# Kernel tuning notes

Hardware: AMD Instinct MI355X
Metric: run time of the kernel (lower is better)

Reference implementation:

```python
import jax, jax.numpy as jnp
import numpy as np

HASH_BINS = 100000
EMB = 64
B = 262144


def _glorot(key, shape):
    fan_in, fan_out = shape[0], shape[-1]
    std = np.sqrt(2.0 / (fan_in + fan_out)).astype(np.float32)
    return jax.random.normal(key, shape, dtype=jnp.float32) * std


def setup_inputs() -> dict:
    key = jax.random.key(0)
    ks = jax.random.split(key, 16)
    return {
        "user_idx": jax.random.randint(ks[0], (B,), 0, HASH_BINS, dtype=jnp.int32),
        "item_idx": jax.random.randint(ks[1], (B,), 0, HASH_BINS, dtype=jnp.int32),
        "user_emb": jax.random.normal(ks[2], (HASH_BINS, EMB), dtype=jnp.float32) * 0.05,
        "item_emb": jax.random.normal(ks[3], (HASH_BINS, EMB), dtype=jnp.float32) * 0.05,
        "lin_w": jax.random.normal(ks[4], (2 * HASH_BINS,), dtype=jnp.float32) * 0.01,
        "lin_b": jnp.zeros((1,), jnp.float32),
        "cross_k": _glorot(ks[5], (2 * EMB, 2 * EMB)),
        "W1": _glorot(ks[6], (2 * EMB, 200)), "b1": jnp.zeros((200,), jnp.float32),
        "W2": _glorot(ks[7], (200, 256)),     "b2": jnp.zeros((256,), jnp.float32),
        "W3": _glorot(ks[8], (256, 200)),     "b3": jnp.zeros((200,), jnp.float32),
        "W4": _glorot(ks[9], (200, 128)),     "b4": jnp.zeros((128,), jnp.float32),
        "W5": _glorot(ks[10], (128, 1)),      "b5": jnp.zeros((1,), jnp.float32),
    }


def reference(user_idx, item_idx, user_emb, item_emb, lin_w, lin_b, cross_k,
              W1, b1, W2, b2, W3, b3, W4, b4, W5, b5):
    # Embedding lookups (flattened + concatenated): [B, 2*EMB]
    emb = jnp.concatenate([user_emb[user_idx], item_emb[item_idx]], axis=1)

    # FM linear term. CategoryEncoding(multi-hot over 2*HASH_BINS) -> Dense(1)
    # is exactly a gather-sum of the dense kernel rows (one user + one item token).
    linear = (lin_w[user_idx] + lin_w[HASH_BINS + item_idx] + lin_b)[:, None]  # [B,1]

    # FM cross term: 0.5 * mean((xK)^2 - x^2 K^2, axis=1)
    xk = emb @ cross_k                      # [B, 128]
    x2k2 = (emb * emb) @ (cross_k * cross_k)
    cross = 0.5 * jnp.mean(xk * xk - x2k2, axis=1, keepdims=True)  # [B,1]

    # Deep MLP (inference: no dropout)
    h = jax.nn.relu(emb @ W1 + b1)
    h = jax.nn.relu(h @ W2 + b2)
    h = jax.nn.relu(h @ W3 + b3)
    h = jax.nn.relu(h @ W4 + b4)
    dnn = h @ W5 + b5                       # [B,1]

    return jax.nn.sigmoid(linear + cross + dnn)
```

## Files before the change

kernel.cpp:

```cpp
#include <hip/hip_runtime.h>

#define HASH_BINS 100000
#define EMBD 64
#define BATCH 262144
#define BM 64
#define SA 264
#define SB 232

typedef __attribute__((ext_vector_type(8))) short short8;
typedef __attribute__((ext_vector_type(4))) float floatx4;
typedef __attribute__((ext_vector_type(4))) unsigned short ushortx4;

static __device__ __forceinline__ unsigned short f2bf(float f) {
  unsigned u = __builtin_bit_cast(unsigned, f);
  u += 0x7fff + ((u >> 16) & 1);
  return (unsigned short)(u >> 16);
}
static __device__ __forceinline__ float bf2f(unsigned short b) {
  return __builtin_bit_cast(float, ((unsigned)b) << 16);
}

__global__ void dfm_prep(const float* __restrict__ K, const float* __restrict__ W1,
                         const float* __restrict__ W2, const float* __restrict__ W3,
                         const float* __restrict__ W4,
                         float* __restrict__ S, unsigned short* __restrict__ Kt,
                         unsigned short* __restrict__ W1t, unsigned short* __restrict__ W2t,
                         unsigned short* __restrict__ W3t, unsigned short* __restrict__ W4t)
{
  int i = blockIdx.x * 256 + threadIdx.x;
  if (i < 4096) {
    int n = i >> 5, k4 = (i & 31) * 4;
    ushortx4 h = { f2bf(K[(k4 + 0) * 128 + n]), f2bf(K[(k4 + 1) * 128 + n]),
                   f2bf(K[(k4 + 2) * 128 + n]), f2bf(K[(k4 + 3) * 128 + n]) };
    *(ushortx4*)&Kt[n * 128 + k4] = h;
  } else if ((i -= 4096) < 7168) {
    int n = i >> 5, k4 = (i & 31) * 4;
    ushortx4 h;
#pragma unroll
    for (int j = 0; j < 4; j++) h[j] = (n < 200) ? f2bf(W1[(k4 + j) * 200 + n]) : 0;
    *(ushortx4*)&W1t[n * 128 + k4] = h;
  } else if ((i -= 7168) < 14336) {
    int n = i / 56, k4 = (i - n * 56) * 4;
    ushortx4 h;
#pragma unroll
    for (int j = 0; j < 4; j++) h[j] = (k4 + j < 200) ? f2bf(W2[(k4 + j) * 256 + n]) : 0;
    *(ushortx4*)&W2t[n * 224 + k4] = h;
  } else if ((i -= 14336) < 14336) {
    int n = i >> 6, k4 = (i & 63) * 4;
    ushortx4 h;
#pragma unroll
    for (int j = 0; j < 4; j++) h[j] = (n < 200) ? f2bf(W3[(k4 + j) * 200 + n]) : 0;
    *(ushortx4*)&W3t[n * 256 + k4] = h;
  } else if ((i -= 14336) < 7168) {
    int n = i / 56, k4 = (i - n * 56) * 4;
    ushortx4 h;
#pragma unroll
    for (int j = 0; j < 4; j++) h[j] = (k4 + j < 200) ? f2bf(W4[(k4 + j) * 128 + n]) : 0;
    *(ushortx4*)&W4t[n * 224 + k4] = h;
  } else if ((i -= 7168) < 128) {
    float s = 0.f;
    for (int j = 0; j < 128; j++) { float v = K[i * 128 + j]; s += v * v; }
    S[i] = s;
  }
}

template <int KP, int CH>
static __device__ __forceinline__ void wpref(const unsigned short* __restrict__ wt,
                                             int tileRow0, int m, int qd, short8* wpre)
{
#pragma unroll
  for (int n = 0; n < CH; n++)
    wpre[n] = *(const short8*)&wt[(tileRow0 + n * 16 + m) * KP + qd * 8];
}

template <int KP, int CH>
static __device__ __forceinline__ void mfma_pass_pre(const unsigned short* __restrict__ wt,
                                                     int tileRow0, const unsigned short* actIn,
                                                     int sin, int m, int qd, floatx4* acc,
                                                     const short8* wpre)
{
#pragma unroll
  for (int i = 0; i < CH * 4; i++) acc[i] = {0.f, 0.f, 0.f, 0.f};
  short8 a[4];
#pragma unroll
  for (int rt = 0; rt < 4; rt++)
    a[rt] = *(const short8*)&actIn[(rt * 16 + m) * sin + qd * 8];
#pragma unroll
  for (int n = 0; n < CH; n++)
#pragma unroll
    for (int rt = 0; rt < 4; rt++)
      acc[n * 4 + rt] = __builtin_amdgcn_mfma_f32_16x16x32_bf16(wpre[n], a[rt], acc[n * 4 + rt], 0, 0, 0);
#pragma unroll
  for (int ks = 1; ks < KP / 32; ks++) {
#pragma unroll
    for (int rt = 0; rt < 4; rt++)
      a[rt] = *(const short8*)&actIn[(rt * 16 + m) * sin + ks * 32 + qd * 8];
#pragma unroll
    for (int n = 0; n < CH; n++) {
      short8 w = *(const short8*)&wt[(tileRow0 + n * 16 + m) * KP + ks * 32 + qd * 8];
#pragma unroll
      for (int rt = 0; rt < 4; rt++)
        acc[n * 4 + rt] = __builtin_amdgcn_mfma_f32_16x16x32_bf16(w, a[rt], acc[n * 4 + rt], 0, 0, 0);
    }
  }
}

template <int KP, int CH>
static __device__ __forceinline__ void mfma_pass(const unsigned short* __restrict__ wt,
                                                 int tileRow0, const unsigned short* actIn,
                                                 int sin, int m, int qd, floatx4* acc)
{
#pragma unroll
  for (int i = 0; i < CH * 4; i++) acc[i] = {0.f, 0.f, 0.f, 0.f};
#pragma unroll
  for (int ks = 0; ks < KP / 32; ks++) {
    short8 a[4];
#pragma unroll
    for (int rt = 0; rt < 4; rt++)
      a[rt] = *(const short8*)&actIn[(rt * 16 + m) * sin + ks * 32 + qd * 8];
#pragma unroll
    for (int n = 0; n < CH; n++) {
      short8 w = *(const short8*)&wt[(tileRow0 + n * 16 + m) * KP + ks * 32 + qd * 8];
#pragma unroll
      for (int rt = 0; rt < 4; rt++)
        acc[n * 4 + rt] = __builtin_amdgcn_mfma_f32_16x16x32_bf16(w, a[rt], acc[n * 4 + rt], 0, 0, 0);
    }
  }
}

template <int CH>
static __device__ __forceinline__ void epilogue_relu(const float* __restrict__ bias,
                                                     int colBase, int nreal,
                                                     unsigned short* actOut, int sout,
                                                     int m, int qd, const floatx4* acc)
{
#pragma unroll
  for (int n = 0; n < CH; n++) {
    int col = colBase + n * 16 + qd * 4;
    float b0 = 0.f, b1 = 0.f, b2 = 0.f, b3 = 0.f;
    if (col < nreal) {
      float4 q = *(const float4*)(bias + col);
      b0 = q.x; b1 = q.y; b2 = q.z; b3 = q.w;
    }
#pragma unroll
    for (int rt = 0; rt < 4; rt++) {
      ushortx4 h = { f2bf(fmaxf(acc[n * 4 + rt][0] + b0, 0.f)),
                     f2bf(fmaxf(acc[n * 4 + rt][1] + b1, 0.f)),
                     f2bf(fmaxf(acc[n * 4 + rt][2] + b2, 0.f)),
                     f2bf(fmaxf(acc[n * 4 + rt][3] + b3, 0.f)) };
      *(ushortx4*)&actOut[(rt * 16 + m) * sout + col] = h;
    }
  }
}

__global__ __launch_bounds__(512)
void dfm_main(const int* __restrict__ uidx, const int* __restrict__ iidx,
              const float* __restrict__ uemb, const float* __restrict__ iemb,
              const float* __restrict__ linw, const float* __restrict__ linb,
              const float* __restrict__ b1, const float* __restrict__ b2,
              const float* __restrict__ b3, const float* __restrict__ b4,
              const float* __restrict__ W5, const float* __restrict__ b5,
              const float* __restrict__ S, const unsigned short* __restrict__ Wc,
              const unsigned short* __restrict__ W2t, const unsigned short* __restrict__ W3t,
              const unsigned short* __restrict__ W4t,
              float* __restrict__ out)
{
  __shared__ unsigned short actA[BM * SA];
  __shared__ unsigned short actB[BM * SB];
  __shared__ float crosspart[4][BM];
  __shared__ float part[BM][8];
  __shared__ float qpart[BM][8];
  __shared__ float linrow[BM];

  const int t = threadIdx.x;
  const int lane = t & 63, wave = t >> 6;
  const int m = lane & 15, qd = lane >> 4;
  const int r = t >> 3, c = t & 7;

  {
    int g = blockIdx.x * BM + r;
    int u = uidx[g], it = iidx[g];
    const float* up = uemb + (long)u * EMBD + c * 8;
    const float* ip = iemb + (long)it * EMBD + c * 8;
    float qp = 0.f;
#pragma unroll
    for (int j = 0; j < 8; j += 4) {
      float4 f = *(const float4*)(up + j);
      int col = c * 8 + j;
      float4 sv = *(const float4*)(S + col);
      ushortx4 h = {f2bf(f.x), f2bf(f.y), f2bf(f.z), f2bf(f.w)};
      *(ushortx4*)&actA[r * SA + col] = h;
      qp += f.x * f.x * sv.x + f.y * f.y * sv.y + f.z * f.z * sv.z + f.w * f.w * sv.w;
    }
#pragma unroll
    for (int j = 0; j < 8; j += 4) {
      float4 f = *(const float4*)(ip + j);
      int col = 64 + c * 8 + j;
      float4 sv = *(const float4*)(S + col);
      ushortx4 h = {f2bf(f.x), f2bf(f.y), f2bf(f.z), f2bf(f.w)};
      *(ushortx4*)&actA[r * SA + col] = h;
      qp += f.x * f.x * sv.x + f.y * f.y * sv.y + f.z * f.z * sv.z + f.w * f.w * sv.w;
    }
    qpart[r][c] = qp;
    if (c == 0) linrow[r] = linw[u] + linw[HASH_BINS + it] + linb[0];
  }

  short8 wpre[3];
  if (wave < 4)      wpref<128, 2>(Wc, 2 * wave * 16, m, qd, wpre);
  else if (wave < 6) wpref<128, 3>(Wc, 128 + (4 + (wave - 4) * 3) * 16, m, qd, wpre);
  else               wpref<128, 2>(Wc, 128 + (10 + (wave - 6) * 2) * 16, m, qd, wpre);
  __syncthreads();

  if (wave < 4) {
    floatx4 acc[8];
    mfma_pass_pre<128, 2>(Wc, 2 * wave * 16, actA, SA, m, qd, acc, wpre);
    float s[4];
#pragma unroll
    for (int rt = 0; rt < 4; rt++) {
      s[rt] = 0.f;
#pragma unroll
      for (int n = 0; n < 2; n++)
#pragma unroll
        for (int i = 0; i < 4; i++)
          s[rt] += acc[n * 4 + rt][i] * acc[n * 4 + rt][i];
      s[rt] += __shfl_xor(s[rt], 16, 64);
      s[rt] += __shfl_xor(s[rt], 32, 64);
    }
    if (qd == 0)
#pragma unroll
      for (int rt = 0; rt < 4; rt++)
        crosspart[wave][rt * 16 + m] = s[rt];
    floatx4 acc2[4];
    mfma_pass<128, 1>(Wc, 128 + wave * 16, actA, SA, m, qd, acc2);
    epilogue_relu<1>(b1, wave * 16, 200, actB, SB, m, qd, acc2);
  } else if (wave < 6) {
    int s0 = 4 + (wave - 4) * 3;
    floatx4 acc[12];
    mfma_pass_pre<128, 3>(Wc, 128 + s0 * 16, actA, SA, m, qd, acc, wpre);
    epilogue_relu<3>(b1, s0 * 16, 200, actB, SB, m, qd, acc);
  } else {
    int s0 = 10 + (wave - 6) * 2;
    floatx4 acc[8];
    mfma_pass_pre<128, 2>(Wc, 128 + s0 * 16, actA, SA, m, qd, acc, wpre);
    epilogue_relu<2>(b1, s0 * 16, 200, actB, SB, m, qd, acc);
  }
  wpref<224, 2>(W2t, wave * 32, m, qd, wpre);
  __syncthreads();

  {
    floatx4 acc[8];
    mfma_pass_pre<224, 2>(W2t, wave * 32, actB, SB, m, qd, acc, wpre);
    epilogue_relu<2>(b2, wave * 32, 256, actA, SA, m, qd, acc);
  }
  if (wave < 6) wpref<256, 2>(W3t, wave * 32, m, qd, wpre);
  else          wpref<256, 1>(W3t, (12 + (wave - 6)) * 16, m, qd, wpre);
  __syncthreads();

  if (wave < 6) {
    floatx4 acc[8];
    mfma_pass_pre<256, 2>(W3t, wave * 32, actA, SA, m, qd, acc, wpre);
    epilogue_relu<2>(b3, wave * 32, 200, actB, SB, m, qd, acc);
  } else {
    int s0 = (12 + (wave - 6)) * 16;
    floatx4 acc[4];
    mfma_pass_pre<256, 1>(W3t, s0, actA, SA, m, qd, acc, wpre);
    epilogue_relu<1>(b3, s0, 200, actB, SB, m, qd, acc);
  }
  wpref<224, 1>(W4t, wave * 16, m, qd, wpre);
  __syncthreads();

  {
    floatx4 acc[4];
    mfma_pass_pre<224, 1>(W4t, wave * 16, actB, SB, m, qd, acc, wpre);
    int nb = wave * 16 + qd * 4;
    float4 w5q = *(const float4*)(W5 + nb);
    float4 b4q = *(const float4*)(b4 + nb);
#pragma unroll
    for (int rt = 0; rt < 4; rt++) {
      float s = fmaxf(acc[rt][0] + b4q.x, 0.f) * w5q.x +
                fmaxf(acc[rt][1] + b4q.y, 0.f) * w5q.y +
                fmaxf(acc[rt][2] + b4q.z, 0.f) * w5q.z +
                fmaxf(acc[rt][3] + b4q.w, 0.f) * w5q.w;
      s += __shfl_xor(s, 16, 64);
      s += __shfl_xor(s, 32, 64);
      if (qd == 0) part[rt * 16 + m][wave] = s;
    }
  }
  __syncthreads();

  if (t < BM) {
    int rr = t;
    float xk2 = crosspart[0][rr] + crosspart[1][rr] + crosspart[2][rr] + crosspart[3][rr];
    float qs = qpart[rr][0] + qpart[rr][1] + qpart[rr][2] + qpart[rr][3] +
               qpart[rr][4] + qpart[rr][5] + qpart[rr][6] + qpart[rr][7];
    float dnn = part[rr][0] + part[rr][1] + part[rr][2] + part[rr][3] +
                part[rr][4] + part[rr][5] + part[rr][6] + part[rr][7];
    const float inv = 0.5f / 128.f;
    float logit = linrow[rr] + inv * (xk2 - qs) + dnn + b5[0];
    out[blockIdx.x * BM + rr] = 1.f / (1.f + expf(-logit));
  }
}

extern "C" void kernel_launch(void* const* d_in, const int* in_sizes, int n_in,
                              void* d_out, int out_size, void* d_ws, size_t ws_size,
                              hipStream_t stream)
{
  const int*   uidx = (const int*)d_in[0];
  const int*   iidx = (const int*)d_in[1];
  const float* uemb = (const float*)d_in[2];
  const float* iemb = (const float*)d_in[3];
  const float* linw = (const float*)d_in[4];
  const float* linb = (const float*)d_in[5];
  const float* K    = (const float*)d_in[6];
  const float* W1   = (const float*)d_in[7];
  const float* b1   = (const float*)d_in[8];
  const float* W2   = (const float*)d_in[9];
  const float* b2   = (const float*)d_in[10];
  const float* W3   = (const float*)d_in[11];
  const float* b3   = (const float*)d_in[12];
  const float* W4   = (const float*)d_in[13];
  const float* b4   = (const float*)d_in[14];
  const float* W5   = (const float*)d_in[15];
  const float* b5   = (const float*)d_in[16];

  char* w = (char*)d_ws;
  float* S = (float*)w;
  unsigned short* Kt  = (unsigned short*)(w + 512);
  unsigned short* W1t = (unsigned short*)(w + 33280);
  unsigned short* W2t = (unsigned short*)(w + 90624);
  unsigned short* W3t = (unsigned short*)(w + 205312);
  unsigned short* W4t = (unsigned short*)(w + 320000);
  float* out = (float*)d_out;

  dfm_prep<<<185, 256, 0, stream>>>(K, W1, W2, W3, W4, S, Kt, W1t, W2t, W3t, W4t);
  dfm_main<<<BATCH / BM, 512, 0, stream>>>(uidx, iidx, uemb, iemb, linw, linb,
                                           b1, b2, b3, b4, W5, b5,
                                           S, Kt, W2t, W3t, W4t, out);
}
```

Before: 278.4 us.

## Halve block to 256 threads and reuse one in-place LDS activation buffer

Each 64-row block now runs on 4 waves instead of 8, and every wave covers twice as many output columns per layer. The two ping-pong LDS activation buffers become one, which is overwritten in place: each layer computes into registers, waits at a barrier, then writes its ReLU outputs back. The goal is lower LDS use per block and more resident blocks per CU (launch bounds 256,4), so more blocks can overlap. In exchange each wave holds more accumulators and does longer serial MFMA work, the extra barriers add sync cost, and register pressure may rise.

```diff
diff --git a/kernel.cpp b/kernel.cpp
--- a/kernel.cpp
+++ b/kernel.cpp
@@ -5,7 +5,6 @@
 #define BATCH 262144
 #define BM 64
 #define SA 264
-#define SB 232
 
 typedef __attribute__((ext_vector_type(8))) short short8;
 typedef __attribute__((ext_vector_type(4))) float floatx4;
@@ -15,9 +14,6 @@
   unsigned u = __builtin_bit_cast(unsigned, f);
   u += 0x7fff + ((u >> 16) & 1);
   return (unsigned short)(u >> 16);
-}
-static __device__ __forceinline__ float bf2f(unsigned short b) {
-  return __builtin_bit_cast(float, ((unsigned)b) << 16);
 }
 
 __global__ void dfm_prep(const float* __restrict__ K, const float* __restrict__ W1,
@@ -76,7 +72,7 @@
 template <int KP, int CH>
 static __device__ __forceinline__ void mfma_pass_pre(const unsigned short* __restrict__ wt,
                                                      int tileRow0, const unsigned short* actIn,
-                                                     int sin, int m, int qd, floatx4* acc,
+                                                     int m, int qd, floatx4* acc,
                                                      const short8* wpre)
 {
 #pragma unroll
@@ -84,7 +80,7 @@
   short8 a[4];
 #pragma unroll
   for (int rt = 0; rt < 4; rt++)
-    a[rt] = *(const short8*)&actIn[(rt * 16 + m) * sin + qd * 8];
+    a[rt] = *(const short8*)&actIn[(rt * 16 + m) * SA + qd * 8];
 #pragma unroll
   for (int n = 0; n < CH; n++)
 #pragma unroll
@@ -94,7 +90,7 @@
   for (int ks = 1; ks < KP / 32; ks++) {
 #pragma unroll
     for (int rt = 0; rt < 4; rt++)
-      a[rt] = *(const short8*)&actIn[(rt * 16 + m) * sin + ks * 32 + qd * 8];
+      a[rt] = *(const short8*)&actIn[(rt * 16 + m) * SA + ks * 32 + qd * 8];
 #pragma unroll
     for (int n = 0; n < CH; n++) {
       short8 w = *(const short8*)&wt[(tileRow0 + n * 16 + m) * KP + ks * 32 + qd * 8];
@@ -108,7 +104,7 @@
 template <int KP, int CH>
 static __device__ __forceinline__ void mfma_pass(const unsigned short* __restrict__ wt,
                                                  int tileRow0, const unsigned short* actIn,
-                                                 int sin, int m, int qd, floatx4* acc)
+                                                 int m, int qd, floatx4* acc)
 {
 #pragma unroll
   for (int i = 0; i < CH * 4; i++) acc[i] = {0.f, 0.f, 0.f, 0.f};
@@ -117,7 +113,7 @@
     short8 a[4];
 #pragma unroll
     for (int rt = 0; rt < 4; rt++)
-      a[rt] = *(const short8*)&actIn[(rt * 16 + m) * sin + ks * 32 + qd * 8];
+      a[rt] = *(const short8*)&actIn[(rt * 16 + m) * SA + ks * 32 + qd * 8];
 #pragma unroll
     for (int n = 0; n < CH; n++) {
       short8 w = *(const short8*)&wt[(tileRow0 + n * 16 + m) * KP + ks * 32 + qd * 8];
@@ -131,7 +127,7 @@
 template <int CH>
 static __device__ __forceinline__ void epilogue_relu(const float* __restrict__ bias,
                                                      int colBase, int nreal,
-                                                     unsigned short* actOut, int sout,
+                                                     unsigned short* act,
                                                      int m, int qd, const floatx4* acc)
 {
 #pragma unroll
@@ -148,12 +144,12 @@
                      f2bf(fmaxf(acc[n * 4 + rt][1] + b1, 0.f)),
                      f2bf(fmaxf(acc[n * 4 + rt][2] + b2, 0.f)),
                      f2bf(fmaxf(acc[n * 4 + rt][3] + b3, 0.f)) };
-      *(ushortx4*)&actOut[(rt * 16 + m) * sout + col] = h;
-    }
-  }
-}
-
-__global__ __launch_bounds__(512)
+      *(ushortx4*)&act[(rt * 16 + m) * SA + col] = h;
+    }
+  }
+}
+
+__global__ __launch_bounds__(256, 4)
 void dfm_main(const int* __restrict__ uidx, const int* __restrict__ iidx,
               const float* __restrict__ uemb, const float* __restrict__ iemb,
               const float* __restrict__ linw, const float* __restrict__ linb,
@@ -165,55 +161,56 @@
               const unsigned short* __restrict__ W4t,
               float* __restrict__ out)
 {
-  __shared__ unsigned short actA[BM * SA];
-  __shared__ unsigned short actB[BM * SB];
+  __shared__ unsigned short act[BM * SA];
   __shared__ float crosspart[4][BM];
-  __shared__ float part[BM][8];
-  __shared__ float qpart[BM][8];
+  __shared__ float part[BM][4];
+  __shared__ float qrow[BM];
   __shared__ float linrow[BM];
 
   const int t = threadIdx.x;
   const int lane = t & 63, wave = t >> 6;
   const int m = lane & 15, qd = lane >> 4;
-  const int r = t >> 3, c = t & 7;
+  const int r = t >> 2, c = t & 3;
+  const int off = (wave < 2) ? wave * 4 : 8 + (wave - 2) * 3;
 
   {
     int g = blockIdx.x * BM + r;
     int u = uidx[g], it = iidx[g];
-    const float* up = uemb + (long)u * EMBD + c * 8;
-    const float* ip = iemb + (long)it * EMBD + c * 8;
+    const float* up = uemb + (long)u * EMBD + c * 16;
+    const float* ip = iemb + (long)it * EMBD + c * 16;
     float qp = 0.f;
 #pragma unroll
-    for (int j = 0; j < 8; j += 4) {
+    for (int j = 0; j < 16; j += 4) {
       float4 f = *(const float4*)(up + j);
-      int col = c * 8 + j;
+      int col = c * 16 + j;
       float4 sv = *(const float4*)(S + col);
       ushortx4 h = {f2bf(f.x), f2bf(f.y), f2bf(f.z), f2bf(f.w)};
-      *(ushortx4*)&actA[r * SA + col] = h;
+      *(ushortx4*)&act[r * SA + col] = h;
       qp += f.x * f.x * sv.x + f.y * f.y * sv.y + f.z * f.z * sv.z + f.w * f.w * sv.w;
     }
 #pragma unroll
-    for (int j = 0; j < 8; j += 4) {
+    for (int j = 0; j < 16; j += 4) {
       float4 f = *(const float4*)(ip + j);
-      int col = 64 + c * 8 + j;
+      int col = 64 + c * 16 + j;
       float4 sv = *(const float4*)(S + col);
       ushortx4 h = {f2bf(f.x), f2bf(f.y), f2bf(f.z), f2bf(f.w)};
-      *(ushortx4*)&actA[r * SA + col] = h;
+      *(ushortx4*)&act[r * SA + col] = h;
       qp += f.x * f.x * sv.x + f.y * f.y * sv.y + f.z * f.z * sv.z + f.w * f.w * sv.w;
     }
-    qpart[r][c] = qp;
-    if (c == 0) linrow[r] = linw[u] + linw[HASH_BINS + it] + linb[0];
-  }
-
-  short8 wpre[3];
-  if (wave < 4)      wpref<128, 2>(Wc, 2 * wave * 16, m, qd, wpre);
-  else if (wave < 6) wpref<128, 3>(Wc, 128 + (4 + (wave - 4) * 3) * 16, m, qd, wpre);
-  else               wpref<128, 2>(Wc, 128 + (10 + (wave - 6) * 2) * 16, m, qd, wpre);
-  __syncthreads();
-
-  if (wave < 4) {
-    floatx4 acc[8];
-    mfma_pass_pre<128, 2>(Wc, 2 * wave * 16, actA, SA, m, qd, acc, wpre);
+    qp += __shfl_xor(qp, 1, 64);
+    qp += __shfl_xor(qp, 2, 64);
+    if (c == 0) {
+      qrow[r] = qp;
+      linrow[r] = linw[u] + linw[HASH_BINS + it] + linb[0];
+    }
+  }
+  short8 wpre[2];
+  wpref<128, 2>(Wc, 2 * wave * 16, m, qd, wpre);
+  __syncthreads();
+
+  {
+    floatx4 accC[8];
+    mfma_pass_pre<128, 2>(Wc, 2 * wave * 16, act, m, qd, accC, wpre);
     float s[4];
 #pragma unroll
     for (int rt = 0; rt < 4; rt++) {
@@ -222,7 +219,7 @@
       for (int n = 0; n < 2; n++)
 #pragma unroll
         for (int i = 0; i < 4; i++)
-          s[rt] += acc[n * 4 + rt][i] * acc[n * 4 + rt][i];
+          s[rt] += accC[n * 4 + rt][i] * accC[n * 4 + rt][i];
       s[rt] += __shfl_xor(s[rt], 16, 64);
       s[rt] += __shfl_xor(s[rt], 32, 64);
     }
@@ -230,57 +227,73 @@
 #pragma unroll
       for (int rt = 0; rt < 4; rt++)
         crosspart[wave][rt * 16 + m] = s[rt];
-    floatx4 acc2[4];
-    mfma_pass<128, 1>(Wc, 128 + wave * 16, actA, SA, m, qd, acc2);
-    epilogue_relu<1>(b1, wave * 16, 200, actB, SB, m, qd, acc2);
-  } else if (wave < 6) {
-    int s0 = 4 + (wave - 4) * 3;
-    floatx4 acc[12];
-    mfma_pass_pre<128, 3>(Wc, 128 + s0 * 16, actA, SA, m, qd, acc, wpre);
-    epilogue_relu<3>(b1, s0 * 16, 200, actB, SB, m, qd, acc);
-  } else {
-    int s0 = 10 + (wave - 6) * 2;
+
+    floatx4 acc1[8];
+    mfma_pass<128, 2>(Wc, 128 + off * 16, act, m, qd, acc1);
+    if (wave < 2) {
+      floatx4 acc2[8];
+      mfma_pass<128, 2>(Wc, 128 + (off + 2) * 16, act, m, qd, acc2);
+      __syncthreads();
+      epilogue_relu<2>(b1, off * 16, 200, act, m, qd, acc1);
+      epilogue_relu<2>(b1, (off + 2) * 16, 200, act, m, qd, acc2);
+    } else {
+      floatx4 acc2[4];
+      mfma_pass<128, 1>(Wc, 128 + (off + 2) * 16, act, m, qd, acc2);
+      __syncthreads();
+      epilogue_relu<2>(b1, off * 16, 200, act, m, qd, acc1);
+      epilogue_relu<1>(b1, (off + 2) * 16, 200, act, m, qd, acc2);
+    }
+  }
+  wpref<224, 2>(W2t, wave * 64, m, qd, wpre);
+  __syncthreads();
+
+  {
+    floatx4 acc1[8], acc2[8];
+    mfma_pass_pre<224, 2>(W2t, wave * 64, act, m, qd, acc1, wpre);
+    mfma_pass<224, 2>(W2t, wave * 64 + 32, act, m, qd, acc2);
+    __syncthreads();
+    epilogue_relu<2>(b2, wave * 64, 256, act, m, qd, acc1);
+    epilogue_relu<2>(b2, wave * 64 + 32, 256, act, m, qd, acc2);
+  }
+  wpref<256, 2>(W3t, off * 16, m, qd, wpre);
+  __syncthreads();
+
+  {
+    floatx4 acc1[8];
+    mfma_pass_pre<256, 2>(W3t, off * 16, act, m, qd, acc1, wpre);
+    if (wave < 2) {
+      floatx4 acc2[8];
+      mfma_pass<256, 2>(W3t, (off + 2) * 16, act, m, qd, acc2);
+      __syncthreads();
+      epilogue_relu<2>(b3, off * 16, 200, act, m, qd, acc1);
+      epilogue_relu<2>(b3, (off + 2) * 16, 200, act, m, qd, acc2);
+    } else {
+      floatx4 acc2[4];
+      mfma_pass<256, 1>(W3t, (off + 2) * 16, act, m, qd, acc2);
+      __syncthreads();
+      epilogue_relu<2>(b3, off * 16, 200, act, m, qd, acc1);
+      epilogue_relu<1>(b3, (off + 2) * 16, 200, act, m, qd, acc2);
+    }
+  }
+  wpref<224, 2>(W4t, wave * 32, m, qd, wpre);
+  __syncthreads();
+
+  {
     floatx4 acc[8];
-    mfma_pass_pre<128, 2>(Wc, 128 + s0 * 16, actA, SA, m, qd, acc, wpre);
-    epilogue_relu<2>(b1, s0 * 16, 200, actB, SB, m, qd, acc);
-  }
-  wpref<224, 2>(W2t, wave * 32, m, qd, wpre);
-  __syncthreads();
-
-  {
-    floatx4 acc[8];
-    mfma_pass_pre<224, 2>(W2t, wave * 32, actB, SB, m, qd, acc, wpre);
-    epilogue_relu<2>(b2, wave * 32, 256, actA, SA, m, qd, acc);
-  }
-  if (wave < 6) wpref<256, 2>(W3t, wave * 32, m, qd, wpre);
-  else          wpref<256, 1>(W3t, (12 + (wave - 6)) * 16, m, qd, wpre);
-  __syncthreads();
-
-  if (wave < 6) {
-    floatx4 acc[8];
-    mfma_pass_pre<256, 2>(W3t, wave * 32, actA, SA, m, qd, acc, wpre);
-    epilogue_relu<2>(b3, wave * 32, 200, actB, SB, m, qd, acc);
-  } else {
-    int s0 = (12 + (wave - 6)) * 16;
-    floatx4 acc[4];
-    mfma_pass_pre<256, 1>(W3t, s0, actA, SA, m, qd, acc, wpre);
-    epilogue_relu<1>(b3, s0, 200, actB, SB, m, qd, acc);
-  }
-  wpref<224, 1>(W4t, wave * 16, m, qd, wpre);
-  __syncthreads();
-
-  {
-    floatx4 acc[4];
-    mfma_pass_pre<224, 1>(W4t, wave * 16, actB, SB, m, qd, acc, wpre);
-    int nb = wave * 16 + qd * 4;
-    float4 w5q = *(const float4*)(W5 + nb);
-    float4 b4q = *(const float4*)(b4 + nb);
+    mfma_pass_pre<224, 2>(W4t, wave * 32, act, m, qd, acc, wpre);
 #pragma unroll
     for (int rt = 0; rt < 4; rt++) {
-      float s = fmaxf(acc[rt][0] + b4q.x, 0.f) * w5q.x +
-                fmaxf(acc[rt][1] + b4q.y, 0.f) * w5q.y +
-                fmaxf(acc[rt][2] + b4q.z, 0.f) * w5q.z +
-                fmaxf(acc[rt][3] + b4q.w, 0.f) * w5q.w;
+      float s = 0.f;
+#pragma unroll
+      for (int n = 0; n < 2; n++) {
+        int nb = wave * 32 + n * 16 + qd * 4;
+        float4 w5q = *(const float4*)(W5 + nb);
+        float4 b4q = *(const float4*)(b4 + nb);
+        s += fmaxf(acc[n * 4 + rt][0] + b4q.x, 0.f) * w5q.x +
+             fmaxf(acc[n * 4 + rt][1] + b4q.y, 0.f) * w5q.y +
+             fmaxf(acc[n * 4 + rt][2] + b4q.z, 0.f) * w5q.z +
+             fmaxf(acc[n * 4 + rt][3] + b4q.w, 0.f) * w5q.w;
+      }
       s += __shfl_xor(s, 16, 64);
       s += __shfl_xor(s, 32, 64);
       if (qd == 0) part[rt * 16 + m][wave] = s;
@@ -289,15 +302,11 @@
   __syncthreads();
 
   if (t < BM) {
-    int rr = t;
-    float xk2 = crosspart[0][rr] + crosspart[1][rr] + crosspart[2][rr] + crosspart[3][rr];
-    float qs = qpart[rr][0] + qpart[rr][1] + qpart[rr][2] + qpart[rr][3] +
-               qpart[rr][4] + qpart[rr][5] + qpart[rr][6] + qpart[rr][7];
-    float dnn = part[rr][0] + part[rr][1] + part[rr][2] + part[rr][3] +
-                part[rr][4] + part[rr][5] + part[rr][6] + part[rr][7];
+    float xk2 = crosspart[0][t] + crosspart[1][t] + crosspart[2][t] + crosspart[3][t];
+    float dnn = part[t][0] + part[t][1] + part[t][2] + part[t][3];
     const float inv = 0.5f / 128.f;
-    float logit = linrow[rr] + inv * (xk2 - qs) + dnn + b5[0];
-    out[blockIdx.x * BM + rr] = 1.f / (1.f + expf(-logit));
+    float logit = linrow[t] + inv * (xk2 - qrow[t]) + dnn + b5[0];
+    out[blockIdx.x * BM + t] = 1.f / (1.f + expf(-logit));
   }
 }
 
@@ -333,7 +342,7 @@
   float* out = (float*)d_out;
 
   dfm_prep<<<185, 256, 0, stream>>>(K, W1, W2, W3, W4, S, Kt, W1t, W2t, W3t, W4t);
-  dfm_main<<<BATCH / BM, 512, 0, stream>>>(uidx, iidx, uemb, iemb, linw, linb,
+  dfm_main<<<BATCH / BM, 256, 0, stream>>>(uidx, iidx, uemb, iemb, linw, linb,
                                            b1, b2, b3, b4, W5, b5,
                                            S, Kt, W2t, W3t, W4t, out);
 }
```

New measurement: 363.9 us. +30.7%, slower.
